# Kernel tuning notes

Hardware: AMD Instinct MI355X
Metric: run time of the kernel (lower is better)

## Reference

```python
import jax, jax.numpy as jnp
import numpy as np

B, H, S, D = 2, 16, 2048, 64
DROPOUT_RATE = 0.1
NEG = -1000000000.0


def setup_inputs() -> dict:
    k = jax.random.key(0)
    kq, kk, kv, km = jax.random.split(k, 4)
    return {
        "query": jax.random.normal(kq, (B, H, S, D), dtype=jnp.float32),
        "key": jax.random.normal(kk, (B, H, S, D), dtype=jnp.float32),
        "value": jax.random.normal(kv, (B, H, S, D), dtype=jnp.float32),
        "mask": jax.random.randint(km, (B, 1, 1, S), 0, 2, dtype=jnp.int32),
    }


def reference(query, key, value, mask):
    d_k = query.shape[-1]
    # scores: [B,H,S,S]
    scores = jnp.einsum("bhqd,bhkd->bhqk", query, key) / jnp.sqrt(
        jnp.asarray(d_k, query.dtype))
    scores = jnp.where(mask == 0, jnp.asarray(NEG, scores.dtype), scores)
    p_attn = jax.nn.softmax(scores, axis=-1)
    # dropout (train mode, inverted scaling) with a fixed key for determinism
    keep = jax.random.bernoulli(jax.random.key(42), 1.0 - DROPOUT_RATE,
                                p_attn.shape)
    p_attn = jnp.where(keep, p_attn / (1.0 - DROPOUT_RATE), 0.0).astype(
        p_attn.dtype)
    out = jnp.einsum("bhqk,bhkd->bhqd", p_attn, value)
    return (out, p_attn)
```

## Files before the change

kernel.cpp:

```cpp
#include <hip/hip_runtime.h>
#include <stdint.h>

#define H_N 16
#define S_N 2048
#define D_N 64
#define QB  64
#define KT  64

typedef __attribute__((ext_vector_type(8))) __bf16 bf16x8;
typedef __attribute__((ext_vector_type(4))) float f32x4;

__device__ __forceinline__ unsigned short f2bf(float f) {
  uint32_t u = __float_as_uint(f);
  u += 0x7FFFu + ((u >> 16) & 1u);
  return (unsigned short)(u >> 16);
}

__device__ __forceinline__ uint2 tf2x32(uint32_t c0, uint32_t c1) {
  const uint32_t K0 = 0u, K1 = 42u, K2 = 0x1BD11BDAu ^ 42u;
  uint32_t x0 = c0 + K0, x1 = c1 + K1;
#define TFR(r) x0 += x1; x1 = __builtin_rotateleft32(x1, r); x1 ^= x0;
  TFR(13) TFR(15) TFR(26) TFR(6)
  x0 += K1; x1 += K2 + 1u;
  TFR(17) TFR(29) TFR(16) TFR(24)
  x0 += K2; x1 += K0 + 2u;
  TFR(13) TFR(15) TFR(26) TFR(6)
  x0 += K0; x1 += K1 + 3u;
  TFR(17) TFR(29) TFR(16) TFR(24)
  x0 += K1; x1 += K2 + 4u;
  TFR(13) TFR(15) TFR(26) TFR(6)
  x0 += K2; x1 += K0 + 5u;
#undef TFR
  return make_uint2(x0, x1);
}

__device__ __forceinline__ bool keep_bit(uint32_t j) {
  uint2 o = tf2x32(0u, j);
  return (((o.x ^ o.y) >> 9) < 0x733333u);
}

__device__ __forceinline__ void stageTile(const float* __restrict__ g,
                                          unsigned short* __restrict__ lds, int tid) {
  const int row = tid >> 2;
  const int c4  = tid & 3;
  const float4* s = (const float4*)(g + (tid << 4));
  float4 a = s[0], b = s[1], c = s[2], d = s[3];
  uint4 q0, q1;
  q0.x = (uint32_t)f2bf(a.x) | ((uint32_t)f2bf(a.y) << 16);
  q0.y = (uint32_t)f2bf(a.z) | ((uint32_t)f2bf(a.w) << 16);
  q0.z = (uint32_t)f2bf(b.x) | ((uint32_t)f2bf(b.y) << 16);
  q0.w = (uint32_t)f2bf(b.z) | ((uint32_t)f2bf(b.w) << 16);
  q1.x = (uint32_t)f2bf(c.x) | ((uint32_t)f2bf(c.y) << 16);
  q1.y = (uint32_t)f2bf(c.z) | ((uint32_t)f2bf(c.w) << 16);
  q1.z = (uint32_t)f2bf(d.x) | ((uint32_t)f2bf(d.y) << 16);
  q1.w = (uint32_t)f2bf(d.z) | ((uint32_t)f2bf(d.w) << 16);
  const int rs = row & 7;
  *(uint4*)&lds[row * 64 + (((c4 * 2)     ^ rs) << 3)] = q0;
  *(uint4*)&lds[row * 64 + (((c4 * 2 + 1) ^ rs) << 3)] = q1;
}

__device__ __forceinline__ void stageTileT(const float* __restrict__ g,
                                           unsigned short* __restrict__ lds, int tid) {
  const int key = tid >> 2;
  const int c4  = tid & 3;
  const float4* s = (const float4*)(g + (tid << 4));
  float4 v0 = s[0], v1 = s[1], v2 = s[2], v3 = s[3];
  const int kc = key >> 3, ke = key & 7;
#define WRT(e, val) { const int dd = c4 * 16 + (e); \
    lds[dd * 64 + (((kc ^ (dd & 7)) << 3) | ke)] = f2bf(val); }
  WRT(0,  v0.x) WRT(1,  v0.y) WRT(2,  v0.z) WRT(3,  v0.w)
  WRT(4,  v1.x) WRT(5,  v1.y) WRT(6,  v1.z) WRT(7,  v1.w)
  WRT(8,  v2.x) WRT(9,  v2.y) WRT(10, v2.z) WRT(11, v2.w)
  WRT(12, v3.x) WRT(13, v3.y) WRT(14, v3.z) WRT(15, v3.w)
#undef WRT
}

__global__ __launch_bounds__(256, 2)
void attn_fused(const float* __restrict__ Q, const float* __restrict__ K,
                const float* __restrict__ V, const int* __restrict__ mask,
                float* __restrict__ outO, float* __restrict__ outP) {
  __shared__ uint4 smemRaw[4096];
  unsigned short* const sbase = (unsigned short*)smemRaw;
  unsigned short* const sQ[2] = {sbase,          sbase + 4096};
  unsigned short* const sK[2] = {sbase + 8192,   sbase + 12288};
  unsigned short* const sV[2] = {sbase + 16384,  sbase + 20480};
  unsigned short* const sP[2] = {sbase + 24576,  sbase + 28672};

  const int tid = threadIdx.x;
  const int l   = tid & 63;
  const int w   = tid >> 6;
  const int h   = blockIdx.x & (H_N - 1);
  const int qt  = blockIdx.x >> 4;
  const int qBase = qt * QB;

  const int lrow = l & 15;
  const int lq4  = l >> 4;

  const size_t base0 = (size_t)h * (S_N * D_N);
  const size_t base1 = (size_t)(H_N + h) * (S_N * D_N);

  stageTile(Q + base0 + (size_t)qBase * D_N, sQ[0], tid);
  stageTile(Q + base1 + (size_t)qBase * D_N, sQ[1], tid);
  __syncthreads();

  bf16x8 qf[2][2];
  {
    const int qrow = w * 16 + lrow;
#pragma unroll
    for (int b = 0; b < 2; ++b)
#pragma unroll
      for (int ks = 0; ks < 2; ++ks) {
        const int cc = ks * 4 + lq4;
        qf[b][ks] = *(const bf16x8*)&sQ[b][qrow * 64 + ((cc ^ (qrow & 7)) << 3)];
      }
  }

  float invl[2][4];
  {
    float lsum[2][4] = {{0.f,0.f,0.f,0.f},{0.f,0.f,0.f,0.f}};
    for (int kt = 0; kt < S_N / KT; ++kt) {
      __syncthreads();
      stageTile(K + base0 + (size_t)(kt * KT) * D_N, sK[0], tid);
      stageTile(K + base1 + (size_t)(kt * KT) * D_N, sK[1], tid);
      __syncthreads();
#pragma unroll
      for (int b = 0; b < 2; ++b) {
#pragma unroll
        for (int n = 0; n < 4; ++n) {
          const int krow = n * 16 + lrow;
          f32x4 acc = {0.f, 0.f, 0.f, 0.f};
#pragma unroll
          for (int ks = 0; ks < 2; ++ks) {
            const int cc = ks * 4 + lq4;
            bf16x8 kf = *(const bf16x8*)&sK[b][krow * 64 + ((cc ^ (krow & 7)) << 3)];
            acc = __builtin_amdgcn_mfma_f32_16x16x32_bf16(qf[b][ks], kf, acc, 0, 0, 0);
          }
          const float mf = (float)mask[b * S_N + kt * KT + krow];
#pragma unroll
          for (int r = 0; r < 4; ++r)
            lsum[b][r] += mf * __expf(acc[r] * 0.125f - 20.0f);
        }
      }
    }
#pragma unroll
    for (int b = 0; b < 2; ++b)
#pragma unroll
      for (int r = 0; r < 4; ++r) {
        float v = lsum[b][r];
        v += __shfl_xor(v, 1);
        v += __shfl_xor(v, 2);
        v += __shfl_xor(v, 4);
        v += __shfl_xor(v, 8);
        invl[b][r] = (v > 0.f) ? (1.0f / v) : 0.f;
      }
  }

  f32x4 oacc[2][4];
#pragma unroll
  for (int b = 0; b < 2; ++b)
#pragma unroll
    for (int n = 0; n < 4; ++n)
      oacc[b][n] = (f32x4){0.f, 0.f, 0.f, 0.f};

  const uint32_t qg = (uint32_t)(qBase + w * 16 + lq4 * 4);

  for (int kt = 0; kt < S_N / KT; ++kt) {
    __syncthreads();
    stageTile (K + base0 + (size_t)(kt * KT) * D_N, sK[0], tid);
    stageTile (K + base1 + (size_t)(kt * KT) * D_N, sK[1], tid);
    stageTileT(V + base0 + (size_t)(kt * KT) * D_N, sV[0], tid);
    stageTileT(V + base1 + (size_t)(kt * KT) * D_N, sV[1], tid);
    __syncthreads();

#pragma unroll
    for (int b = 0; b < 2; ++b) {
#pragma unroll
      for (int n = 0; n < 4; ++n) {
        const int krow = n * 16 + lrow;
        f32x4 acc = {0.f, 0.f, 0.f, 0.f};
#pragma unroll
        for (int ks = 0; ks < 2; ++ks) {
          const int cc = ks * 4 + lq4;
          bf16x8 kf = *(const bf16x8*)&sK[b][krow * 64 + ((cc ^ (krow & 7)) << 3)];
          acc = __builtin_amdgcn_mfma_f32_16x16x32_bf16(qf[b][ks], kf, acc, 0, 0, 0);
        }
        const int kg = kt * KT + krow;
        const float mf = (float)mask[b * S_N + kg];
        const size_t pBase = (size_t)(b * H_N + h) * (size_t)(S_N * S_N);
        const uint32_t j0 = (uint32_t)(b * H_N + h) * 4194304u + qg * 2048u + (uint32_t)kg;
#pragma unroll
        for (int r = 0; r < 4; ++r) {
          const float p = mf * __expf(acc[r] * 0.125f - 20.0f) * invl[b][r];
          const bool keep = keep_bit(j0 + (uint32_t)r * 2048u);
          const float pd = keep ? p * (1.0f / 0.9f) : 0.0f;
          __builtin_nontemporal_store(pd, &outP[pBase + (size_t)(qg + r) * S_N + (size_t)kg]);
          const int prow = w * 16 + lq4 * 4 + r;
          sP[b][prow * 64 + ((((krow >> 3) ^ (prow & 7)) << 3) | (krow & 7))] = f2bf(pd);
        }
      }
#pragma unroll
      for (int ks = 0; ks < 2; ++ks) {
        const int cc = ks * 4 + lq4;
        const int prow = w * 16 + lrow;
        bf16x8 af = *(const bf16x8*)&sP[b][prow * 64 + ((cc ^ (prow & 7)) << 3)];
#pragma unroll
        for (int n = 0; n < 4; ++n) {
          const int vrow = n * 16 + lrow;
          bf16x8 vf = *(const bf16x8*)&sV[b][vrow * 64 + ((cc ^ (vrow & 7)) << 3)];
          oacc[b][n] = __builtin_amdgcn_mfma_f32_16x16x32_bf16(af, vf, oacc[b][n], 0, 0, 0);
        }
      }
    }
  }

#pragma unroll
  for (int b = 0; b < 2; ++b)
#pragma unroll
    for (int n = 0; n < 4; ++n)
#pragma unroll
      for (int r = 0; r < 4; ++r) {
        const size_t off = ((size_t)(b * H_N + h) * S_N + (size_t)(qg + r)) * D_N + n * 16 + lrow;
        __builtin_nontemporal_store(oacc[b][n][r], &outO[off]);
      }
}

extern "C" void kernel_launch(void* const* d_in, const int* in_sizes, int n_in,
                              void* d_out, int out_size, void* d_ws, size_t ws_size,
                              hipStream_t stream) {
  const float* Q   = (const float*)d_in[0];
  const float* K   = (const float*)d_in[1];
  const float* V   = (const float*)d_in[2];
  const int* mask  = (const int*)d_in[3];
  float* outO = (float*)d_out;
  float* outP = outO + (size_t)2 * H_N * S_N * D_N;
  hipLaunchKernelGGL(attn_fused, dim3(512), dim3(256), 0, stream,
                     Q, K, V, mask, outO, outP);
}
```

Baseline: 408.0 us.

## Split batch across blocks to double grid and halve LDS per block

Each block now handles one batch element instead of both, so the grid doubles to 1024 blocks while LDS and register use per block are halved. Launch bounds rise to 4 blocks per CU to raise occupancy. The dropout scale is folded into the inverse row sum to save one multiply per element. In exchange, the two batch elements no longer share a block, and the tighter launch bounds may cause register spilling.

```diff
diff --git a/kernel.cpp b/kernel.cpp
--- a/kernel.cpp
+++ b/kernel.cpp
@@ -75,105 +75,52 @@
 #undef WRT
 }
 
-__global__ __launch_bounds__(256, 2)
+__global__ __launch_bounds__(256, 4)
 void attn_fused(const float* __restrict__ Q, const float* __restrict__ K,
                 const float* __restrict__ V, const int* __restrict__ mask,
                 float* __restrict__ outO, float* __restrict__ outP) {
-  __shared__ uint4 smemRaw[4096];
+  __shared__ uint4 smemRaw[2048];
   unsigned short* const sbase = (unsigned short*)smemRaw;
-  unsigned short* const sQ[2] = {sbase,          sbase + 4096};
-  unsigned short* const sK[2] = {sbase + 8192,   sbase + 12288};
-  unsigned short* const sV[2] = {sbase + 16384,  sbase + 20480};
-  unsigned short* const sP[2] = {sbase + 24576,  sbase + 28672};
+  unsigned short* const sQ = sbase;
+  unsigned short* const sK = sbase + 4096;
+  unsigned short* const sV = sbase + 8192;
+  unsigned short* const sP = sbase + 12288;
 
   const int tid = threadIdx.x;
   const int l   = tid & 63;
   const int w   = tid >> 6;
-  const int h   = blockIdx.x & (H_N - 1);
-  const int qt  = blockIdx.x >> 4;
+  const int bid = blockIdx.x;
+  const int b   = bid & 1;
+  const int h   = (bid >> 1) & (H_N - 1);
+  const int qt  = bid >> 5;
   const int qBase = qt * QB;
 
   const int lrow = l & 15;
   const int lq4  = l >> 4;
 
-  const size_t base0 = (size_t)h * (S_N * D_N);
-  const size_t base1 = (size_t)(H_N + h) * (S_N * D_N);
-
-  stageTile(Q + base0 + (size_t)qBase * D_N, sQ[0], tid);
-  stageTile(Q + base1 + (size_t)qBase * D_N, sQ[1], tid);
+  const size_t base = ((size_t)b * H_N + h) * (size_t)(S_N * D_N);
+  const int* const maskRow = mask + b * S_N;
+
+  stageTile(Q + base + (size_t)qBase * D_N, sQ, tid);
   __syncthreads();
 
-  bf16x8 qf[2][2];
+  bf16x8 qf[2];
   {
     const int qrow = w * 16 + lrow;
 #pragma unroll
-    for (int b = 0; b < 2; ++b)
-#pragma unroll
-      for (int ks = 0; ks < 2; ++ks) {
-        const int cc = ks * 4 + lq4;
-        qf[b][ks] = *(const bf16x8*)&sQ[b][qrow * 64 + ((cc ^ (qrow & 7)) << 3)];
-      }
+    for (int ks = 0; ks < 2; ++ks) {
+      const int cc = ks * 4 + lq4;
+      qf[ks] = *(const bf16x8*)&sQ[qrow * 64 + ((cc ^ (qrow & 7)) << 3)];
+    }
   }
 
-  float invl[2][4];
+  float minv[4];
   {
-    float lsum[2][4] = {{0.f,0.f,0.f,0.f},{0.f,0.f,0.f,0.f}};
+    float lsum[4] = {0.f, 0.f, 0.f, 0.f};
     for (int kt = 0; kt < S_N / KT; ++kt) {
       __syncthreads();
-      stageTile(K + base0 + (size_t)(kt * KT) * D_N, sK[0], tid);
-      stageTile(K + base1 + (size_t)(kt * KT) * D_N, sK[1], tid);
+      stageTile(K + base + (size_t)(kt * KT) * D_N, sK, tid);
       __syncthreads();
-#pragma unroll
-      for (int b = 0; b < 2; ++b) {
-#pragma unroll
-        for (int n = 0; n < 4; ++n) {
-          const int krow = n * 16 + lrow;
-          f32x4 acc = {0.f, 0.f, 0.f, 0.f};
-#pragma unroll
-          for (int ks = 0; ks < 2; ++ks) {
-            const int cc = ks * 4 + lq4;
-            bf16x8 kf = *(const bf16x8*)&sK[b][krow * 64 + ((cc ^ (krow & 7)) << 3)];
-            acc = __builtin_amdgcn_mfma_f32_16x16x32_bf16(qf[b][ks], kf, acc, 0, 0, 0);
-          }
-          const float mf = (float)mask[b * S_N + kt * KT + krow];
-#pragma unroll
-          for (int r = 0; r < 4; ++r)
-            lsum[b][r] += mf * __expf(acc[r] * 0.125f - 20.0f);
-        }
-      }
-    }
-#pragma unroll
-    for (int b = 0; b < 2; ++b)
-#pragma unroll
-      for (int r = 0; r < 4; ++r) {
-        float v = lsum[b][r];
-        v += __shfl_xor(v, 1);
-        v += __shfl_xor(v, 2);
-        v += __shfl_xor(v, 4);
-        v += __shfl_xor(v, 8);
-        invl[b][r] = (v > 0.f) ? (1.0f / v) : 0.f;
-      }
-  }
-
-  f32x4 oacc[2][4];
-#pragma unroll
-  for (int b = 0; b < 2; ++b)
-#pragma unroll
-    for (int n = 0; n < 4; ++n)
-      oacc[b][n] = (f32x4){0.f, 0.f, 0.f, 0.f};
-
-  const uint32_t qg = (uint32_t)(qBase + w * 16 + lq4 * 4);
-
-  for (int kt = 0; kt < S_N / KT; ++kt) {
-    __syncthreads();
-    stageTile (K + base0 + (size_t)(kt * KT) * D_N, sK[0], tid);
-    stageTile (K + base1 + (size_t)(kt * KT) * D_N, sK[1], tid);
-    stageTileT(V + base0 + (size_t)(kt * KT) * D_N, sV[0], tid);
-    stageTileT(V + base1 + (size_t)(kt * KT) * D_N, sV[1], tid);
-    __syncthreads();
-
-#pragma unroll
-    for (int b = 0; b < 2; ++b) {
 #pragma unroll
       for (int n = 0; n < 4; ++n) {
         const int krow = n * 16 + lrow;
@@ -181,47 +128,85 @@
 #pragma unroll
         for (int ks = 0; ks < 2; ++ks) {
           const int cc = ks * 4 + lq4;
-          bf16x8 kf = *(const bf16x8*)&sK[b][krow * 64 + ((cc ^ (krow & 7)) << 3)];
-          acc = __builtin_amdgcn_mfma_f32_16x16x32_bf16(qf[b][ks], kf, acc, 0, 0, 0);
+          bf16x8 kf = *(const bf16x8*)&sK[krow * 64 + ((cc ^ (krow & 7)) << 3)];
+          acc = __builtin_amdgcn_mfma_f32_16x16x32_bf16(qf[ks], kf, acc, 0, 0, 0);
         }
-        const int kg = kt * KT + krow;
-        const float mf = (float)mask[b * S_N + kg];
-        const size_t pBase = (size_t)(b * H_N + h) * (size_t)(S_N * S_N);
-        const uint32_t j0 = (uint32_t)(b * H_N + h) * 4194304u + qg * 2048u + (uint32_t)kg;
-#pragma unroll
-        for (int r = 0; r < 4; ++r) {
-          const float p = mf * __expf(acc[r] * 0.125f - 20.0f) * invl[b][r];
-          const bool keep = keep_bit(j0 + (uint32_t)r * 2048u);
-          const float pd = keep ? p * (1.0f / 0.9f) : 0.0f;
-          __builtin_nontemporal_store(pd, &outP[pBase + (size_t)(qg + r) * S_N + (size_t)kg]);
-          const int prow = w * 16 + lq4 * 4 + r;
-          sP[b][prow * 64 + ((((krow >> 3) ^ (prow & 7)) << 3) | (krow & 7))] = f2bf(pd);
-        }
-      }
+        const float mf = (float)maskRow[kt * KT + krow];
+#pragma unroll
+        for (int r = 0; r < 4; ++r)
+          lsum[r] += mf * __expf(acc[r] * 0.125f - 20.0f);
+      }
+    }
+#pragma unroll
+    for (int r = 0; r < 4; ++r) {
+      float v = lsum[r];
+      v += __shfl_xor(v, 1);
+      v += __shfl_xor(v, 2);
+      v += __shfl_xor(v, 4);
+      v += __shfl_xor(v, 8);
+      minv[r] = (v > 0.f) ? ((1.0f / 0.9f) / v) : 0.f;
+    }
+  }
+
+  f32x4 oacc[4];
+#pragma unroll
+  for (int n = 0; n < 4; ++n)
+    oacc[n] = (f32x4){0.f, 0.f, 0.f, 0.f};
+
+  const uint32_t qg = (uint32_t)(qBase + w * 16 + lq4 * 4);
+  const size_t pBase = ((size_t)b * H_N + h) * (size_t)(S_N * S_N);
+  const uint32_t jBase = (uint32_t)(b * H_N + h) * 4194304u + qg * 2048u;
+
+  for (int kt = 0; kt < S_N / KT; ++kt) {
+    __syncthreads();
+    stageTile (K + base + (size_t)(kt * KT) * D_N, sK, tid);
+    stageTileT(V + base + (size_t)(kt * KT) * D_N, sV, tid);
+    __syncthreads();
+
+#pragma unroll
+    for (int n = 0; n < 4; ++n) {
+      const int krow = n * 16 + lrow;
+      f32x4 acc = {0.f, 0.f, 0.f, 0.f};
 #pragma unroll
       for (int ks = 0; ks < 2; ++ks) {
         const int cc = ks * 4 + lq4;
-        const int prow = w * 16 + lrow;
-        bf16x8 af = *(const bf16x8*)&sP[b][prow * 64 + ((cc ^ (prow & 7)) << 3)];
-#pragma unroll
-        for (int n = 0; n < 4; ++n) {
-          const int vrow = n * 16 + lrow;
-          bf16x8 vf = *(const bf16x8*)&sV[b][vrow * 64 + ((cc ^ (vrow & 7)) << 3)];
-          oacc[b][n] = __builtin_amdgcn_mfma_f32_16x16x32_bf16(af, vf, oacc[b][n], 0, 0, 0);
-        }
+        bf16x8 kf = *(const bf16x8*)&sK[krow * 64 + ((cc ^ (krow & 7)) << 3)];
+        acc = __builtin_amdgcn_mfma_f32_16x16x32_bf16(qf[ks], kf, acc, 0, 0, 0);
+      }
+      const int kg = kt * KT + krow;
+      const float mf = (float)maskRow[kg];
+      const uint32_t j0 = jBase + (uint32_t)kg;
+#pragma unroll
+      for (int r = 0; r < 4; ++r) {
+        const float pe = mf * __expf(acc[r] * 0.125f - 20.0f) * minv[r];
+        const bool keep = keep_bit(j0 + (uint32_t)r * 2048u);
+        const float pd = keep ? pe : 0.0f;
+        __builtin_nontemporal_store(pd, &outP[pBase + (size_t)(qg + r) * S_N + (size_t)kg]);
+        const int prow = w * 16 + lq4 * 4 + r;
+        sP[prow * 64 + ((((krow >> 3) ^ (prow & 7)) << 3) | (krow & 7))] = f2bf(pd);
+      }
+    }
+#pragma unroll
+    for (int ks = 0; ks < 2; ++ks) {
+      const int cc = ks * 4 + lq4;
+      const int prow = w * 16 + lrow;
+      bf16x8 af = *(const bf16x8*)&sP[prow * 64 + ((cc ^ (prow & 7)) << 3)];
+#pragma unroll
+      for (int n = 0; n < 4; ++n) {
+        const int vrow = n * 16 + lrow;
+        bf16x8 vf = *(const bf16x8*)&sV[vrow * 64 + ((cc ^ (vrow & 7)) << 3)];
+        oacc[n] = __builtin_amdgcn_mfma_f32_16x16x32_bf16(af, vf, oacc[n], 0, 0, 0);
       }
     }
   }
 
 #pragma unroll
-  for (int b = 0; b < 2; ++b)
-#pragma unroll
-    for (int n = 0; n < 4; ++n)
-#pragma unroll
-      for (int r = 0; r < 4; ++r) {
-        const size_t off = ((size_t)(b * H_N + h) * S_N + (size_t)(qg + r)) * D_N + n * 16 + lrow;
-        __builtin_nontemporal_store(oacc[b][n][r], &outO[off]);
-      }
+  for (int n = 0; n < 4; ++n)
+#pragma unroll
+    for (int r = 0; r < 4; ++r) {
+      const size_t off = (((size_t)b * H_N + h) * S_N + (size_t)(qg + r)) * D_N + n * 16 + lrow;
+      __builtin_nontemporal_store(oacc[n][r], &outO[off]);
+    }
 }
 
 extern "C" void kernel_launch(void* const* d_in, const int* in_sizes, int n_in,
@@ -233,6 +218,6 @@
   const int* mask  = (const int*)d_in[3];
   float* outO = (float*)d_out;
   float* outP = outO + (size_t)2 * H_N * S_N * D_N;
-  hipLaunchKernelGGL(attn_fused, dim3(512), dim3(256), 0, stream,
+  hipLaunchKernelGGL(attn_fused, dim3(1024), dim3(256), 0, stream,
                      Q, K, V, mask, outO, outP);
 }
```

Result: faster. 369.0 us (-9.5%).
